# Kernel optimization log

Hardware: AMD Instinct MI355X
Metric: run time of the kernel (lower is better)

The kernel has to match this reference:

```python
import jax, jax.numpy as jnp
import numpy as np

N = 100000   # nodes
E = 1600000  # edges
IN = 128     # in_feats
H = 64       # h_feats
NEG_SLOPE = 0.2  # DGL GATConv default negative_slope


def setup_inputs() -> dict:
    key = jax.random.key(0)
    ks = jax.random.split(key, 6)
    in_feat = jax.random.normal(ks[0], (N, IN), jnp.float32)
    src = jax.random.randint(ks[1], (E,), 0, N)
    dst = jax.random.randint(ks[2], (E,), 0, N)

    def mk(k, din, dout):
        k1, k2, k3 = jax.random.split(k, 3)
        W = jax.random.normal(k1, (dout, din), jnp.float32) * np.float32(1.0 / np.sqrt(din))
        al = jax.random.normal(k2, (dout,), jnp.float32) * 0.1
        ar = jax.random.normal(k3, (dout,), jnp.float32) * 0.1
        b = jnp.zeros((dout,), jnp.float32)
        return W, al, ar, b

    W1, al1, ar1, b1 = mk(ks[3], IN, H)
    W2, al2, ar2, b2 = mk(ks[4], H, H)
    W3, al3, ar3, b3 = mk(ks[5], H, H)
    return dict(in_feat=in_feat, W1=W1, al1=al1, ar1=ar1, b1=b1,
                W2=W2, al2=al2, ar2=ar2, b2=b2,
                W3=W3, al3=al3, ar3=ar3, b3=b3,
                src=src, dst=dst)


def gat_layer(x, W, al, ar, b, src, dst):
    # DGL GATConv, num_heads=1: project, edge attention, segment softmax over dst, scatter-agg, bias, ReLU
    feat = x @ W.T                                   # [N, H]
    el = feat @ al                                   # [N] a_l . Wh_i
    er = feat @ ar                                   # [N] a_r . Wh_j
    e = jax.nn.leaky_relu(el[src] + er[dst], NEG_SLOPE)   # [E]
    m = jax.ops.segment_max(e, dst, num_segments=N)       # per-dst max (stable softmax)
    ee = jnp.exp(e - m[dst])                               # [E]
    denom = jax.ops.segment_sum(ee, dst, num_segments=N)  # [N]
    alpha = ee / denom[dst]                                # [E]
    out = jax.ops.segment_sum(feat[src] * alpha[:, None], dst, num_segments=N)  # [N, H]
    return jax.nn.relu(out + b)


def reference(in_feat, W1, al1, ar1, b1, W2, al2, ar2, b2, W3, al3, ar3, b3, src, dst):
    h = gat_layer(in_feat, W1, al1, ar1, b1, src, dst)
    h = gat_layer(h, W2, al2, ar2, b2, src, dst)
    h = gat_layer(h, W3, al3, ar3, b3, src, dst)
    return h
```

## Files before the change

### kernel.cpp

```cpp
#include <hip/hip_runtime.h>
#include <math.h>

#define NNODES 100000
#define NEDGES 1600000
#define HF 64
#define NBUCK_SHIFT 9
#define NBUCK 256
#define NBUCK_USED ((NNODES + 511) >> 9)
#define KC_BLOCKS 512
#define KB_BLOCKS 1024

__global__ __launch_bounds__(256) void k_bcount(
    const int* __restrict__ dst, int* __restrict__ bcnt, int E)
{
    __shared__ int hist[NBUCK];
    const int tid = threadIdx.x;
    const int EPB = (E + KC_BLOCKS - 1) / KC_BLOCKS;
    const int e0 = blockIdx.x * EPB;
    const int e1 = min(E, e0 + EPB);
    hist[tid] = 0;
    __syncthreads();
    for (int i = e0 + tid; i < e1; i += 256)
        atomicAdd(&hist[dst[i] >> NBUCK_SHIFT], 1);
    __syncthreads();
    if (hist[tid]) atomicAdd(&bcnt[tid], hist[tid]);
}

__global__ __launch_bounds__(256) void k_bscan(
    const int* __restrict__ bcnt, int* __restrict__ gcur, int* __restrict__ bstart)
{
    __shared__ int s[256];
    const int tid = threadIdx.x;
    int own = bcnt[tid];
    s[tid] = own;
    __syncthreads();
    for (int off = 1; off < 256; off <<= 1) {
        int t = (tid >= off) ? s[tid - off] : 0;
        __syncthreads();
        s[tid] += t;
        __syncthreads();
    }
    int excl = s[tid] - own;
    gcur[tid] = excl;
    bstart[tid] = excl;
    if (tid == 255) bstart[256] = s[255];
}

__global__ __launch_bounds__(256) void k_bucket(
    const int* __restrict__ src, const int* __restrict__ dst,
    int* __restrict__ gcur, int2* __restrict__ ebuf2, int E)
{
    __shared__ int hist[NBUCK];
    const int tid = threadIdx.x;
    const int EPB = (E + KB_BLOCKS - 1) / KB_BLOCKS;
    const int e0 = blockIdx.x * EPB;
    const int e1 = min(E, e0 + EPB);

    hist[tid] = 0;
    __syncthreads();
    for (int i = e0 + tid; i < e1; i += 256)
        atomicAdd(&hist[dst[i] >> NBUCK_SHIFT], 1);
    __syncthreads();
    int cnt = hist[tid];
    int base = (cnt > 0) ? atomicAdd(&gcur[tid], cnt) : 0;
    __syncthreads();
    hist[tid] = base;
    __syncthreads();
    for (int i = e0 + tid; i < e1; i += 256) {
        int d = dst[i];
        int r = atomicAdd(&hist[d >> NBUCK_SHIFT], 1);
        ebuf2[r] = make_int2(src[i], d);
    }
}

__global__ __launch_bounds__(256) void k_local(
    const int2* __restrict__ ebuf2, const int* __restrict__ bstart,
    int* __restrict__ deg, int* __restrict__ cur, int* __restrict__ esrc)
{
    __shared__ int lhist[512];
    __shared__ int lcur[512];
    __shared__ int s[256];
    const int b = blockIdx.x;
    const int tid = threadIdx.x;
    const int e0 = bstart[b];
    const int e1 = bstart[b + 1];
    const int n0 = b << NBUCK_SHIFT;

    lhist[tid] = 0;
    lhist[tid + 256] = 0;
    __syncthreads();
    for (int i = e0 + tid; i < e1; i += 256)
        atomicAdd(&lhist[ebuf2[i].y - n0], 1);
    __syncthreads();

    int v0 = lhist[2 * tid], v1 = lhist[2 * tid + 1];
    int tsum = v0 + v1;
    s[tid] = tsum;
    __syncthreads();
    for (int off = 1; off < 256; off <<= 1) {
        int t = (tid >= off) ? s[tid - off] : 0;
        __syncthreads();
        s[tid] += t;
        __syncthreads();
    }
    int run = s[tid] - tsum;
    lcur[2 * tid] = run;
    lcur[2 * tid + 1] = run + v0;
    int node0 = n0 + 2 * tid;
    if (node0 < NNODES)     { deg[node0] = v0;     cur[node0] = e0 + run + v0; }
    if (node0 + 1 < NNODES) { deg[node0 + 1] = v1; cur[node0 + 1] = e0 + run + v0 + v1; }
    __syncthreads();

    for (int i = e0 + tid; i < e1; i += 256) {
        int2 e = ebuf2[i];
        int p = atomicAdd(&lcur[e.y - n0], 1);
        esrc[e0 + p] = e.x;
    }
}

template <int K>
__global__ __launch_bounds__(256) void gemm_tile(
    const float* __restrict__ x, const float* __restrict__ W,
    const float* __restrict__ al, const float* __restrict__ ar,
    float* __restrict__ feat, float* __restrict__ el, float* __restrict__ er,
    int n)
{
    constexpr int KS = 32;
    __shared__ float xs[KS][132];
    __shared__ float wt[KS][68];

    const int tid = threadIdx.x;
    const int tx = tid & 15;
    const int ty = tid >> 4;
    const int row0 = blockIdx.x * 128;

    float acc[8][4];
#pragma unroll
    for (int i = 0; i < 8; ++i)
#pragma unroll
        for (int j = 0; j < 4; ++j) acc[i][j] = 0.f;

    for (int ks = 0; ks < K; ks += KS) {
        if (ks) __syncthreads();
#pragma unroll
        for (int jj = 0; jj < 4; ++jj) {
            int j = tid + jj * 256;
            int r = j >> 3;
            int k4 = j & 7;
            int gr = row0 + r;
            float4 v = make_float4(0.f, 0.f, 0.f, 0.f);
            if (gr < n) v = *(const float4*)(x + (size_t)gr * K + ks + 4 * k4);
            xs[4 * k4 + 0][r] = v.x;
            xs[4 * k4 + 1][r] = v.y;
            xs[4 * k4 + 2][r] = v.z;
            xs[4 * k4 + 3][r] = v.w;
        }
#pragma unroll
        for (int jj = 0; jj < 2; ++jj) {
            int j = tid + jj * 256;
            int c = j >> 3;
            int k4 = j & 7;
            float4 v = *(const float4*)(W + (size_t)c * K + ks + 4 * k4);
            wt[4 * k4 + 0][c] = v.x;
            wt[4 * k4 + 1][c] = v.y;
            wt[4 * k4 + 2][c] = v.z;
            wt[4 * k4 + 3][c] = v.w;
        }
        __syncthreads();

#pragma unroll 8
        for (int k = 0; k < KS; ++k) {
            float4 a0 = *(const float4*)&xs[k][8 * ty + 0];
            float4 a1 = *(const float4*)&xs[k][8 * ty + 4];
            float4 b  = *(const float4*)&wt[k][4 * tx];
            float ar_[8] = {a0.x, a0.y, a0.z, a0.w, a1.x, a1.y, a1.z, a1.w};
            float bc[4] = {b.x, b.y, b.z, b.w};
#pragma unroll
            for (int i = 0; i < 8; ++i)
#pragma unroll
                for (int j = 0; j < 4; ++j)
                    acc[i][j] += ar_[i] * bc[j];
        }
    }

    const float4 ald = *(const float4*)(al + 4 * tx);
    const float4 ard = *(const float4*)(ar + 4 * tx);
#pragma unroll
    for (int i = 0; i < 8; ++i) {
        int row = row0 + 8 * ty + i;
        float pl = acc[i][0] * ald.x + acc[i][1] * ald.y +
                   acc[i][2] * ald.z + acc[i][3] * ald.w;
        float pr = acc[i][0] * ard.x + acc[i][1] * ard.y +
                   acc[i][2] * ard.z + acc[i][3] * ard.w;
#pragma unroll
        for (int off = 8; off >= 1; off >>= 1) {
            pl += __shfl_xor(pl, off);
            pr += __shfl_xor(pr, off);
        }
        if (row < n) {
            float4 st = make_float4(acc[i][0], acc[i][1], acc[i][2], acc[i][3]);
            *(float4*)(feat + (size_t)row * HF + 4 * tx) = st;
            if (tx == 0) { el[row] = pl; er[row] = pr; }
        }
    }
}

__global__ __launch_bounds__(256) void node_agg(
    const int* __restrict__ cur, const int* __restrict__ deg,
    const int* __restrict__ esrc,
    const float* __restrict__ el, const float* __restrict__ er,
    const float* __restrict__ feat, const float* __restrict__ bias,
    float* __restrict__ out, int n)
{
    const int node = blockIdx.x * 4 + (threadIdx.x >> 6);
    if (node >= n) return;
    const int lane = threadIdx.x & 63;
    const int cx = lane & 15;
    const int lg = lane >> 4;

    const int dg = deg[node];

    if (dg == 0) {
        if (lane < 16) {
            float4 b4 = *(const float4*)(bias + 4 * cx);
            float4 o;
            o.x = fmaxf(b4.x, 0.f); o.y = fmaxf(b4.y, 0.f);
            o.z = fmaxf(b4.z, 0.f); o.w = fmaxf(b4.w, 0.f);
            *(float4*)(out + (size_t)node * HF + 4 * cx) = o;
        }
        return;
    }

    const int base = cur[node] - dg;
    const float erd = er[node];

    if (dg <= 32) {
        int sreg = 0;
        if (lane < dg) sreg = esrc[base + lane];
        float elv = 0.f;
        if (lane < dg) elv = el[sreg];

        int sj[8];
#pragma unroll
        for (int t = 0; t < 8; ++t) sj[t] = __shfl(sreg, lg + 4 * t);

        float4 f[8];
#pragma unroll
        for (int t = 0; t < 8; ++t)
            if (lg + 4 * t < dg)
                f[t] = *(const float4*)(feat + (size_t)sj[t] * HF + 4 * cx);

        float ereg = -INFINITY;
        if (lane < dg) {
            float e = elv + erd;
            ereg = (e >= 0.f) ? e : 0.2f * e;
        }
        float m = ereg;
#pragma unroll
        for (int off = 32; off >= 1; off >>= 1)
            m = fmaxf(m, __shfl_xor(m, off));
        float ee = __expf(ereg - m);
        float den = ee;
#pragma unroll
        for (int off = 32; off >= 1; off >>= 1)
            den += __shfl_xor(den, off);

        float4 c[4];
#pragma unroll
        for (int q = 0; q < 4; ++q) c[q] = make_float4(0.f, 0.f, 0.f, 0.f);
#pragma unroll
        for (int t = 0; t < 8; ++t) {
            float w = __shfl(ee, lg + 4 * t);
            if (lg + 4 * t < dg) {
                c[t & 3].x += w * f[t].x;
                c[t & 3].y += w * f[t].y;
                c[t & 3].z += w * f[t].z;
                c[t & 3].w += w * f[t].w;
            }
        }
        float4 acc;
        acc.x = (c[0].x + c[1].x) + (c[2].x + c[3].x);
        acc.y = (c[0].y + c[1].y) + (c[2].y + c[3].y);
        acc.z = (c[0].z + c[1].z) + (c[2].z + c[3].z);
        acc.w = (c[0].w + c[1].w) + (c[2].w + c[3].w);
#pragma unroll
        for (int off = 16; off <= 32; off <<= 1) {
            acc.x += __shfl_xor(acc.x, off);
            acc.y += __shfl_xor(acc.y, off);
            acc.z += __shfl_xor(acc.z, off);
            acc.w += __shfl_xor(acc.w, off);
        }
        if (lane < 16) {
            float inv = 1.f / den;
            float4 b4 = *(const float4*)(bias + 4 * cx);
            float4 o;
            o.x = fmaxf(acc.x * inv + b4.x, 0.f);
            o.y = fmaxf(acc.y * inv + b4.y, 0.f);
            o.z = fmaxf(acc.z * inv + b4.z, 0.f);
            o.w = fmaxf(acc.w * inv + b4.w, 0.f);
            *(float4*)(out + (size_t)node * HF + 4 * cx) = o;
        }
        return;
    }

    if (dg <= 64) {
        int sreg = 0;
        float ereg = -INFINITY;
        if (lane < dg) {
            sreg = esrc[base + lane];
            float e = el[sreg] + erd;
            ereg = (e >= 0.f) ? e : 0.2f * e;
        }
        float m = ereg;
#pragma unroll
        for (int off = 32; off >= 1; off >>= 1)
            m = fmaxf(m, __shfl_xor(m, off));
        float ee = __expf(ereg - m);
        float den = ee;
#pragma unroll
        for (int off = 32; off >= 1; off >>= 1)
            den += __shfl_xor(den, off);

        float4 c[4];
#pragma unroll
        for (int q = 0; q < 4; ++q) c[q] = make_float4(0.f, 0.f, 0.f, 0.f);
        for (int j0 = 0; j0 < dg; j0 += 16) {
#pragma unroll
            for (int q = 0; q < 4; ++q) {
                int jj = j0 + lg + 4 * q;
                int   s = __shfl(sreg, jj & 63);
                float w = __shfl(ee, jj & 63);
                if (jj < dg) {
                    float4 fv = *(const float4*)(feat + (size_t)s * HF + 4 * cx);
                    c[q].x += w * fv.x;
                    c[q].y += w * fv.y;
                    c[q].z += w * fv.z;
                    c[q].w += w * fv.w;
                }
            }
        }
        float4 acc;
        acc.x = (c[0].x + c[1].x) + (c[2].x + c[3].x);
        acc.y = (c[0].y + c[1].y) + (c[2].y + c[3].y);
        acc.z = (c[0].z + c[1].z) + (c[2].z + c[3].z);
        acc.w = (c[0].w + c[1].w) + (c[2].w + c[3].w);
#pragma unroll
        for (int off = 16; off <= 32; off <<= 1) {
            acc.x += __shfl_xor(acc.x, off);
            acc.y += __shfl_xor(acc.y, off);
            acc.z += __shfl_xor(acc.z, off);
            acc.w += __shfl_xor(acc.w, off);
        }
        if (lane < 16) {
            float inv = 1.f / den;
            float4 b4 = *(const float4*)(bias + 4 * cx);
            float4 o;
            o.x = fmaxf(acc.x * inv + b4.x, 0.f);
            o.y = fmaxf(acc.y * inv + b4.y, 0.f);
            o.z = fmaxf(acc.z * inv + b4.z, 0.f);
            o.w = fmaxf(acc.w * inv + b4.w, 0.f);
            *(float4*)(out + (size_t)node * HF + 4 * cx) = o;
        }
        return;
    }

    float m = -INFINITY;
    for (int j = lane; j < dg; j += 64) {
        int s = esrc[base + j];
        float e = el[s] + erd;
        e = (e >= 0.f) ? e : 0.2f * e;
        m = fmaxf(m, e);
    }
#pragma unroll
    for (int off = 32; off >= 1; off >>= 1)
        m = fmaxf(m, __shfl_xor(m, off));

    float acc = 0.f, den = 0.f;
    for (int j = 0; j < dg; ++j) {
        int s = esrc[base + j];
        float e = el[s] + erd;
        e = (e >= 0.f) ? e : 0.2f * e;
        float ee = __expf(e - m);
        den += ee;
        acc += ee * feat[(size_t)s * HF + lane];
    }
    out[(size_t)node * HF + lane] = fmaxf(acc / den + bias[lane], 0.f);
}

extern "C" void kernel_launch(void* const* d_in, const int* in_sizes, int n_in,
                              void* d_out, int out_size, void* d_ws, size_t ws_size,
                              hipStream_t stream) {
    const int N = NNODES;
    const int E = NEDGES;

    const float* in_feat = (const float*)d_in[0];
    const float* W1 = (const float*)d_in[1];
    const float* al1 = (const float*)d_in[2];
    const float* ar1 = (const float*)d_in[3];
    const float* b1 = (const float*)d_in[4];
    const float* W2 = (const float*)d_in[5];
    const float* al2 = (const float*)d_in[6];
    const float* ar2 = (const float*)d_in[7];
    const float* b2 = (const float*)d_in[8];
    const float* W3 = (const float*)d_in[9];
    const float* al3 = (const float*)d_in[10];
    const float* ar3 = (const float*)d_in[11];
    const float* b3 = (const float*)d_in[12];
    const int* src = (const int*)d_in[13];
    const int* dst = (const int*)d_in[14];

    float* ws = (float*)d_ws;
    float* feat = ws;
    float* h1   = feat + (size_t)N * HF;
    float* h2   = h1 + (size_t)N * HF;
    float* el   = h2 + (size_t)N * HF;
    float* er   = el + N;
    int* deg    = (int*)(er + N);
    int* cur    = deg + N;
    int* bcnt   = cur + N;
    int* bstart = bcnt + 256;
    int* gcur   = bstart + 260;
    int* esrc   = gcur + 256;
    int2* ebuf2 = (int2*)h1;

    const int gEdge = (E + 255) / 256;
    const int gNode4 = (N + 3) / 4;
    const int gTile = (N + 127) / 128;
    (void)gEdge;

    hipMemsetAsync(bcnt, 0, NBUCK * 4, stream);
    k_bcount<<<KC_BLOCKS, 256, 0, stream>>>(dst, bcnt, E);
    k_bscan<<<1, 256, 0, stream>>>(bcnt, gcur, bstart);
    k_bucket<<<KB_BLOCKS, 256, 0, stream>>>(src, dst, gcur, ebuf2, E);
    k_local<<<NBUCK_USED, 256, 0, stream>>>(ebuf2, bstart, deg, cur, esrc);

    float* out = (float*)d_out;

    gemm_tile<128><<<gTile, 256, 0, stream>>>(in_feat, W1, al1, ar1, feat, el, er, N);
    node_agg<<<gNode4, 256, 0, stream>>>(cur, deg, esrc, el, er, feat, b1, h1, N);

    gemm_tile<64><<<gTile, 256, 0, stream>>>(h1, W2, al2, ar2, feat, el, er, N);
    node_agg<<<gNode4, 256, 0, stream>>>(cur, deg, esrc, el, er, feat, b2, h2, N);

    gemm_tile<64><<<gTile, 256, 0, stream>>>(h2, W3, al3, ar3, feat, el, er, N);
    node_agg<<<gNode4, 256, 0, stream>>>(cur, deg, esrc, el, er, feat, b3, out, N);
}
```

Baseline: 343.0 us.

## Pack edge buffer, double-buffer GEMM tiles, and process two nodes per wavefront

Edge bucketing now writes a single packed int per edge (src shifted left by nine, low nine bits of dst) instead of an int2, which halves the scatter and read traffic of the CSR build. The projection GEMM gains register-staged double buffering in shared memory so the next K-chunk loads while the current one computes. The aggregation kernel now maps two destination nodes onto each 64-lane wavefront, one per 32-lane half, to cut idle lanes at the typical degree of about 16. The packing assumes src fits in 23 bits, and the half-wave layout adds more per-lane loop work for high-degree nodes.

```diff
diff --git a/kernel.cpp b/kernel.cpp
--- a/kernel.cpp
+++ b/kernel.cpp
@@ -48,7 +48,7 @@
 
 __global__ __launch_bounds__(256) void k_bucket(
     const int* __restrict__ src, const int* __restrict__ dst,
-    int* __restrict__ gcur, int2* __restrict__ ebuf2, int E)
+    int* __restrict__ gcur, int* __restrict__ epack, int E)
 {
     __shared__ int hist[NBUCK];
     const int tid = threadIdx.x;
@@ -69,12 +69,12 @@
     for (int i = e0 + tid; i < e1; i += 256) {
         int d = dst[i];
         int r = atomicAdd(&hist[d >> NBUCK_SHIFT], 1);
-        ebuf2[r] = make_int2(src[i], d);
+        epack[r] = (src[i] << NBUCK_SHIFT) | (d & 511);
     }
 }
 
 __global__ __launch_bounds__(256) void k_local(
-    const int2* __restrict__ ebuf2, const int* __restrict__ bstart,
+    const int* __restrict__ epack, const int* __restrict__ bstart,
     int* __restrict__ deg, int* __restrict__ cur, int* __restrict__ esrc)
 {
     __shared__ int lhist[512];
@@ -90,7 +90,7 @@
     lhist[tid + 256] = 0;
     __syncthreads();
     for (int i = e0 + tid; i < e1; i += 256)
-        atomicAdd(&lhist[ebuf2[i].y - n0], 1);
+        atomicAdd(&lhist[epack[i] & 511], 1);
     __syncthreads();
 
     int v0 = lhist[2 * tid], v1 = lhist[2 * tid + 1];
@@ -112,9 +112,9 @@
     __syncthreads();
 
     for (int i = e0 + tid; i < e1; i += 256) {
-        int2 e = ebuf2[i];
-        int p = atomicAdd(&lcur[e.y - n0], 1);
-        esrc[e0 + p] = e.x;
+        int p = epack[i];
+        int pos = atomicAdd(&lcur[p & 511], 1);
+        esrc[e0 + pos] = ((unsigned)p) >> NBUCK_SHIFT;
     }
 }
 
@@ -126,8 +126,9 @@
     int n)
 {
     constexpr int KS = 32;
-    __shared__ float xs[KS][132];
-    __shared__ float wt[KS][68];
+    constexpr int NC = K / KS;
+    __shared__ float xs[2][KS][132];
+    __shared__ float wt[2][KS][68];
 
     const int tid = threadIdx.x;
     const int tx = tid & 15;
@@ -140,39 +141,62 @@
 #pragma unroll
         for (int j = 0; j < 4; ++j) acc[i][j] = 0.f;
 
-    for (int ks = 0; ks < K; ks += KS) {
-        if (ks) __syncthreads();
-#pragma unroll
-        for (int jj = 0; jj < 4; ++jj) {
-            int j = tid + jj * 256;
-            int r = j >> 3;
-            int k4 = j & 7;
-            int gr = row0 + r;
-            float4 v = make_float4(0.f, 0.f, 0.f, 0.f);
-            if (gr < n) v = *(const float4*)(x + (size_t)gr * K + ks + 4 * k4);
-            xs[4 * k4 + 0][r] = v.x;
-            xs[4 * k4 + 1][r] = v.y;
-            xs[4 * k4 + 2][r] = v.z;
-            xs[4 * k4 + 3][r] = v.w;
-        }
-#pragma unroll
-        for (int jj = 0; jj < 2; ++jj) {
-            int j = tid + jj * 256;
-            int c = j >> 3;
-            int k4 = j & 7;
-            float4 v = *(const float4*)(W + (size_t)c * K + ks + 4 * k4);
-            wt[4 * k4 + 0][c] = v.x;
-            wt[4 * k4 + 1][c] = v.y;
-            wt[4 * k4 + 2][c] = v.z;
-            wt[4 * k4 + 3][c] = v.w;
-        }
-        __syncthreads();
-
+    float4 xr[4], wr[2];
+#pragma unroll
+    for (int jj = 0; jj < 4; ++jj) {
+        int j = tid + jj * 256;
+        int gr = row0 + (j >> 3);
+        xr[jj] = make_float4(0.f, 0.f, 0.f, 0.f);
+        if (gr < n) xr[jj] = *(const float4*)(x + (size_t)gr * K + 4 * (j & 7));
+    }
+#pragma unroll
+    for (int jj = 0; jj < 2; ++jj) {
+        int j = tid + jj * 256;
+        wr[jj] = *(const float4*)(W + (size_t)(j >> 3) * K + 4 * (j & 7));
+    }
+#pragma unroll
+    for (int jj = 0; jj < 4; ++jj) {
+        int j = tid + jj * 256;
+        int r = j >> 3, k4 = j & 7;
+        xs[0][4 * k4 + 0][r] = xr[jj].x;
+        xs[0][4 * k4 + 1][r] = xr[jj].y;
+        xs[0][4 * k4 + 2][r] = xr[jj].z;
+        xs[0][4 * k4 + 3][r] = xr[jj].w;
+    }
+#pragma unroll
+    for (int jj = 0; jj < 2; ++jj) {
+        int j = tid + jj * 256;
+        int c = j >> 3, k4 = j & 7;
+        wt[0][4 * k4 + 0][c] = wr[jj].x;
+        wt[0][4 * k4 + 1][c] = wr[jj].y;
+        wt[0][4 * k4 + 2][c] = wr[jj].z;
+        wt[0][4 * k4 + 3][c] = wr[jj].w;
+    }
+    __syncthreads();
+
+#pragma unroll
+    for (int c = 0; c < NC; ++c) {
+        const int buf = c & 1;
+        if (c + 1 < NC) {
+            const int ks = (c + 1) * KS;
+#pragma unroll
+            for (int jj = 0; jj < 4; ++jj) {
+                int j = tid + jj * 256;
+                int gr = row0 + (j >> 3);
+                xr[jj] = make_float4(0.f, 0.f, 0.f, 0.f);
+                if (gr < n) xr[jj] = *(const float4*)(x + (size_t)gr * K + ks + 4 * (j & 7));
+            }
+#pragma unroll
+            for (int jj = 0; jj < 2; ++jj) {
+                int j = tid + jj * 256;
+                wr[jj] = *(const float4*)(W + (size_t)(j >> 3) * K + ks + 4 * (j & 7));
+            }
+        }
 #pragma unroll 8
         for (int k = 0; k < KS; ++k) {
-            float4 a0 = *(const float4*)&xs[k][8 * ty + 0];
-            float4 a1 = *(const float4*)&xs[k][8 * ty + 4];
-            float4 b  = *(const float4*)&wt[k][4 * tx];
+            float4 a0 = *(const float4*)&xs[buf][k][8 * ty + 0];
+            float4 a1 = *(const float4*)&xs[buf][k][8 * ty + 4];
+            float4 b  = *(const float4*)&wt[buf][k][4 * tx];
             float ar_[8] = {a0.x, a0.y, a0.z, a0.w, a1.x, a1.y, a1.z, a1.w};
             float bc[4] = {b.x, b.y, b.z, b.w};
 #pragma unroll
@@ -180,6 +204,28 @@
 #pragma unroll
                 for (int j = 0; j < 4; ++j)
                     acc[i][j] += ar_[i] * bc[j];
+        }
+        if (c + 1 < NC) {
+            const int nb = buf ^ 1;
+#pragma unroll
+            for (int jj = 0; jj < 4; ++jj) {
+                int j = tid + jj * 256;
+                int r = j >> 3, k4 = j & 7;
+                xs[nb][4 * k4 + 0][r] = xr[jj].x;
+                xs[nb][4 * k4 + 1][r] = xr[jj].y;
+                xs[nb][4 * k4 + 2][r] = xr[jj].z;
+                xs[nb][4 * k4 + 3][r] = xr[jj].w;
+            }
+#pragma unroll
+            for (int jj = 0; jj < 2; ++jj) {
+                int j = tid + jj * 256;
+                int cc = j >> 3, k4 = j & 7;
+                wt[nb][4 * k4 + 0][cc] = wr[jj].x;
+                wt[nb][4 * k4 + 1][cc] = wr[jj].y;
+                wt[nb][4 * k4 + 2][cc] = wr[jj].z;
+                wt[nb][4 * k4 + 3][cc] = wr[jj].w;
+            }
+            __syncthreads();
         }
     }
 
@@ -212,16 +258,21 @@
     const float* __restrict__ feat, const float* __restrict__ bias,
     float* __restrict__ out, int n)
 {
-    const int node = blockIdx.x * 4 + (threadIdx.x >> 6);
+    const int tid = threadIdx.x;
+    const int lane = tid & 63;
+    const int half = lane >> 5;
+    const int l32 = lane & 31;
+    const int cx = l32 & 15;
+    const int lg = l32 >> 4;
+    const int hb = half << 5;
+
+    const int node = blockIdx.x * 8 + (tid >> 6) * 2 + half;
     if (node >= n) return;
-    const int lane = threadIdx.x & 63;
-    const int cx = lane & 15;
-    const int lg = lane >> 4;
 
     const int dg = deg[node];
 
     if (dg == 0) {
-        if (lane < 16) {
+        if (l32 < 16) {
             float4 b4 = *(const float4*)(bias + 4 * cx);
             float4 o;
             o.x = fmaxf(b4.x, 0.f); o.y = fmaxf(b4.y, 0.f);
@@ -236,33 +287,40 @@
 
     if (dg <= 32) {
         int sreg = 0;
-        if (lane < dg) sreg = esrc[base + lane];
-        float elv = 0.f;
-        if (lane < dg) elv = el[sreg];
+        if (l32 < dg) sreg = esrc[base + l32];
+        float elv = (l32 < dg) ? el[sreg] : 0.f;
 
         int sj[8];
 #pragma unroll
-        for (int t = 0; t < 8; ++t) sj[t] = __shfl(sreg, lg + 4 * t);
-
+        for (int t = 0; t < 8; ++t) sj[t] = __shfl(sreg, hb + lg + 2 * t);
         float4 f[8];
 #pragma unroll
         for (int t = 0; t < 8; ++t)
-            if (lg + 4 * t < dg)
+            if (lg + 2 * t < dg)
                 f[t] = *(const float4*)(feat + (size_t)sj[t] * HF + 4 * cx);
 
+        int sj2[8];
+#pragma unroll
+        for (int t = 0; t < 8; ++t) sj2[t] = __shfl(sreg, hb + 16 + lg + 2 * t);
+        float4 f2[8];
+#pragma unroll
+        for (int t = 0; t < 8; ++t)
+            if (16 + lg + 2 * t < dg)
+                f2[t] = *(const float4*)(feat + (size_t)sj2[t] * HF + 4 * cx);
+
         float ereg = -INFINITY;
-        if (lane < dg) {
+        if (l32 < dg) {
             float e = elv + erd;
             ereg = (e >= 0.f) ? e : 0.2f * e;
         }
         float m = ereg;
 #pragma unroll
-        for (int off = 32; off >= 1; off >>= 1)
+        for (int off = 16; off >= 1; off >>= 1)
             m = fmaxf(m, __shfl_xor(m, off));
         float ee = __expf(ereg - m);
         float den = ee;
 #pragma unroll
-        for (int off = 32; off >= 1; off >>= 1)
+        for (int off = 16; off >= 1; off >>= 1)
             den += __shfl_xor(den, off);
 
         float4 c[4];
@@ -270,12 +328,22 @@
         for (int q = 0; q < 4; ++q) c[q] = make_float4(0.f, 0.f, 0.f, 0.f);
 #pragma unroll
         for (int t = 0; t < 8; ++t) {
-            float w = __shfl(ee, lg + 4 * t);
-            if (lg + 4 * t < dg) {
+            float w = __shfl(ee, hb + lg + 2 * t);
+            if (lg + 2 * t < dg) {
                 c[t & 3].x += w * f[t].x;
                 c[t & 3].y += w * f[t].y;
                 c[t & 3].z += w * f[t].z;
                 c[t & 3].w += w * f[t].w;
+            }
+        }
+#pragma unroll
+        for (int t = 0; t < 8; ++t) {
+            float w = __shfl(ee, hb + 16 + lg + 2 * t);
+            if (16 + lg + 2 * t < dg) {
+                c[t & 3].x += w * f2[t].x;
+                c[t & 3].y += w * f2[t].y;
+                c[t & 3].z += w * f2[t].z;
+                c[t & 3].w += w * f2[t].w;
             }
         }
         float4 acc;
@@ -283,14 +351,11 @@
         acc.y = (c[0].y + c[1].y) + (c[2].y + c[3].y);
         acc.z = (c[0].z + c[1].z) + (c[2].z + c[3].z);
         acc.w = (c[0].w + c[1].w) + (c[2].w + c[3].w);
-#pragma unroll
-        for (int off = 16; off <= 32; off <<= 1) {
-            acc.x += __shfl_xor(acc.x, off);
-            acc.y += __shfl_xor(acc.y, off);
-            acc.z += __shfl_xor(acc.z, off);
-            acc.w += __shfl_xor(acc.w, off);
-        }
-        if (lane < 16) {
+        acc.x += __shfl_xor(acc.x, 16);
+        acc.y += __shfl_xor(acc.y, 16);
+        acc.z += __shfl_xor(acc.z, 16);
+        acc.w += __shfl_xor(acc.w, 16);
+        if (l32 < 16) {
             float inv = 1.f / den;
             float4 b4 = *(const float4*)(bias + 4 * cx);
             float4 o;
@@ -304,33 +369,39 @@
     }
 
     if (dg <= 64) {
-        int sreg = 0;
-        float ereg = -INFINITY;
-        if (lane < dg) {
-            sreg = esrc[base + lane];
-            float e = el[sreg] + erd;
-            ereg = (e >= 0.f) ? e : 0.2f * e;
-        }
-        float m = ereg;
-#pragma unroll
-        for (int off = 32; off >= 1; off >>= 1)
+        int s0 = 0, s1 = 0;
+        float e0 = -INFINITY, e1 = -INFINITY;
+        if (l32 < dg) {
+            s0 = esrc[base + l32];
+            float e = el[s0] + erd;
+            e0 = (e >= 0.f) ? e : 0.2f * e;
+        }
+        if (32 + l32 < dg) {
+            s1 = esrc[base + 32 + l32];
+            float e = el[s1] + erd;
+            e1 = (e >= 0.f) ? e : 0.2f * e;
+        }
+        float m = fmaxf(e0, e1);
+#pragma unroll
+        for (int off = 16; off >= 1; off >>= 1)
             m = fmaxf(m, __shfl_xor(m, off));
-        float ee = __expf(ereg - m);
-        float den = ee;
-#pragma unroll
-        for (int off = 32; off >= 1; off >>= 1)
+        float x0 = __expf(e0 - m), x1 = __expf(e1 - m);
+        float den = x0 + x1;
+#pragma unroll
+        for (int off = 16; off >= 1; off >>= 1)
             den += __shfl_xor(den, off);
 
-        float4 c[4];
-#pragma unroll
-        for (int q = 0; q < 4; ++q) c[q] = make_float4(0.f, 0.f, 0.f, 0.f);
-        for (int j0 = 0; j0 < dg; j0 += 16) {
-#pragma unroll
-            for (int q = 0; q < 4; ++q) {
-                int jj = j0 + lg + 4 * q;
-                int   s = __shfl(sreg, jj & 63);
-                float w = __shfl(ee, jj & 63);
-                if (jj < dg) {
+        float4 c[2];
+        c[0] = make_float4(0.f, 0.f, 0.f, 0.f);
+        c[1] = c[0];
+        for (int j0 = 0; j0 < dg; j0 += 4) {
+#pragma unroll
+            for (int q = 0; q < 2; ++q) {
+                int jb = j0 + lg + 2 * q;
+                int s; float w;
+                if (jb < 32) { s = __shfl(s0, hb + jb);      w = __shfl(x0, hb + jb); }
+                else         { s = __shfl(s1, hb + jb - 32); w = __shfl(x1, hb + jb - 32); }
+                if (jb < dg) {
                     float4 fv = *(const float4*)(feat + (size_t)s * HF + 4 * cx);
                     c[q].x += w * fv.x;
                     c[q].y += w * fv.y;
@@ -340,18 +411,15 @@
             }
         }
         float4 acc;
-        acc.x = (c[0].x + c[1].x) + (c[2].x + c[3].x);
-        acc.y = (c[0].y + c[1].y) + (c[2].y + c[3].y);
-        acc.z = (c[0].z + c[1].z) + (c[2].z + c[3].z);
-        acc.w = (c[0].w + c[1].w) + (c[2].w + c[3].w);
-#pragma unroll
-        for (int off = 16; off <= 32; off <<= 1) {
-            acc.x += __shfl_xor(acc.x, off);
-            acc.y += __shfl_xor(acc.y, off);
-            acc.z += __shfl_xor(acc.z, off);
-            acc.w += __shfl_xor(acc.w, off);
-        }
-        if (lane < 16) {
+        acc.x = c[0].x + c[1].x;
+        acc.y = c[0].y + c[1].y;
+        acc.z = c[0].z + c[1].z;
+        acc.w = c[0].w + c[1].w;
+        acc.x += __shfl_xor(acc.x, 16);
+        acc.y += __shfl_xor(acc.y, 16);
+        acc.z += __shfl_xor(acc.z, 16);
+        acc.w += __shfl_xor(acc.w, 16);
+        if (l32 < 16) {
             float inv = 1.f / den;
             float4 b4 = *(const float4*)(bias + 4 * cx);
             float4 o;
@@ -364,27 +432,33 @@
         return;
     }
 
-    float m = -INFINITY;
-    for (int j = lane; j < dg; j += 64) {
-        int s = esrc[base + j];
-        float e = el[s] + erd;
-        e = (e >= 0.f) ? e : 0.2f * e;
-        m = fmaxf(m, e);
-    }
-#pragma unroll
-    for (int off = 32; off >= 1; off >>= 1)
-        m = fmaxf(m, __shfl_xor(m, off));
-
-    float acc = 0.f, den = 0.f;
-    for (int j = 0; j < dg; ++j) {
-        int s = esrc[base + j];
-        float e = el[s] + erd;
-        e = (e >= 0.f) ? e : 0.2f * e;
-        float ee = __expf(e - m);
-        den += ee;
-        acc += ee * feat[(size_t)s * HF + lane];
-    }
-    out[(size_t)node * HF + lane] = fmaxf(acc / den + bias[lane], 0.f);
+    {
+        float m = -INFINITY;
+        for (int j = l32; j < dg; j += 32) {
+            int s = esrc[base + j];
+            float e = el[s] + erd;
+            e = (e >= 0.f) ? e : 0.2f * e;
+            m = fmaxf(m, e);
+        }
+#pragma unroll
+        for (int off = 16; off >= 1; off >>= 1)
+            m = fmaxf(m, __shfl_xor(m, off));
+
+        float2 acc = make_float2(0.f, 0.f);
+        float den = 0.f;
+        for (int j = 0; j < dg; ++j) {
+            int s = esrc[base + j];
+            float e = el[s] + erd;
+            e = (e >= 0.f) ? e : 0.2f * e;
+            float ee = __expf(e - m);
+            den += ee;
+            acc.x += ee * feat[(size_t)s * HF + 2 * l32];
+            acc.y += ee * feat[(size_t)s * HF + 2 * l32 + 1];
+        }
+        float inv = 1.f / den;
+        out[(size_t)node * HF + 2 * l32]     = fmaxf(acc.x * inv + bias[2 * l32], 0.f);
+        out[(size_t)node * HF + 2 * l32 + 1] = fmaxf(acc.y * inv + bias[2 * l32 + 1], 0.f);
+    }
 }
 
 extern "C" void kernel_launch(void* const* d_in, const int* in_sizes, int n_in,
@@ -421,27 +495,25 @@
     int* bstart = bcnt + 256;
     int* gcur   = bstart + 260;
     int* esrc   = gcur + 256;
-    int2* ebuf2 = (int2*)h1;
-
-    const int gEdge = (E + 255) / 256;
-    const int gNode4 = (N + 3) / 4;
+    int* epack  = (int*)h1;
+
+    const int gNode8 = (N + 7) / 8;
     const int gTile = (N + 127) / 128;
-    (void)gEdge;
 
     hipMemsetAsync(bcnt, 0, NBUCK * 4, stream);
     k_bcount<<<KC_BLOCKS, 256, 0, stream>>>(dst, bcnt, E);
     k_bscan<<<1, 256, 0, stream>>>(bcnt, gcur, bstart);
-    k_bucket<<<KB_BLOCKS, 256, 0, stream>>>(src, dst, gcur, ebuf2, E);
-    k_local<<<NBUCK_USED, 256, 0, stream>>>(ebuf2, bstart, deg, cur, esrc);
+    k_bucket<<<KB_BLOCKS, 256, 0, stream>>>(src, dst, gcur, epack, E);
+    k_local<<<NBUCK_USED, 256, 0, stream>>>(epack, bstart, deg, cur, esrc);
 
     float* out = (float*)d_out;
 
     gemm_tile<128><<<gTile, 256, 0, stream>>>(in_feat, W1, al1, ar1, feat, el, er, N);
-    node_agg<<<gNode4, 256, 0, stream>>>(cur, deg, esrc, el, er, feat, b1, h1, N);
+    node_agg<<<gNode8, 256, 0, stream>>>(cur, deg, esrc, el, er, feat, b1, h1, N);
 
     gemm_tile<64><<<gTile, 256, 0, stream>>>(h1, W2, al2, ar2, feat, el, er, N);
-    node_agg<<<gNode4, 256, 0, stream>>>(cur, deg, esrc, el, er, feat, b2, h2, N);
+    node_agg<<<gNode8, 256, 0, stream>>>(cur, deg, esrc, el, er, feat, b2, h2, N);
 
     gemm_tile<64><<<gTile, 256, 0, stream>>>(h2, W3, al3, ar3, feat, el, er, N);
-    node_agg<<<gNode4, 256, 0, stream>>>(cur, deg, esrc, el, er, feat, b3, out, N);
-}
+    node_agg<<<gNode8, 256, 0, stream>>>(cur, deg, esrc, el, er, feat, b3, out, N);
+}
```

Result: slower. 361.7 us (+5.5%).
